# Kernel tuning notes

Measured on AMD Instinct MI355X. Metric: run time of the kernel, lower is better.

Reference implementation:

```python
import jax, jax.numpy as jnp
import numpy as np

SIZE = 32
NUM_CLASSES = 10
B = 16384
RTOL = 0.01
ATOL = 0.01
MAX_STEPS = 96
H0 = 0.05


def setup_inputs() -> dict:
    key = jax.random.key(0)
    ks = jax.random.split(key, 9)
    p = lambda k, s: 0.1 * jax.random.normal(k, s, dtype=jnp.float32)
    z = lambda n: jnp.zeros((n,), dtype=jnp.float32)
    x = jax.random.normal(ks[0], (B, 2), dtype=jnp.float32)
    # per-sample ODE end times T_i in (0, 3]
    samples = 3.0 * jax.random.uniform(ks[1], (B, 1), dtype=jnp.float32) + 1e-3
    return dict(
        x=x, samples=samples,
        node_w1=p(ks[2], (3, SIZE)), node_b1=z(SIZE),
        node_w2=p(ks[3], (SIZE, SIZE)), node_b2=z(SIZE),
        node_w3=p(ks[4], (SIZE, 2)), node_b3=z(2),
        fc_w=p(ks[5], (2, NUM_CLASSES)), fc_b=z(NUM_CLASSES),
        enc_w1=p(ks[6], (2, SIZE)), enc_b1=z(SIZE),
        enc_w2=p(ks[7], (SIZE, SIZE)), enc_b2=z(SIZE),
        enc_w3=p(ks[8], (SIZE, 2)), enc_b3=z(2),
    )


def _net_forward(x, samples, node_w1, node_b1, node_w2, node_b2, node_w3, node_b3,
                 fc_w, fc_b, enc_w1, enc_b1, enc_w2, enc_b2, enc_w3, enc_b3):
    # Encoder -> (alpha, beta) feed only the external prob_model (no effect on act_vec)
    h = jax.nn.relu(x @ enc_w1 + enc_b1)
    h = jax.nn.relu(h @ enc_w2 + enc_b2)
    ab = h @ enc_w3 + enc_b3
    alpha, beta = jnp.exp(ab[:, 0]), jnp.exp(ab[:, 1])  # unused downstream (side effects only)

    # samples[samples >= 50] = 50
    T = jnp.minimum(samples[:, 0], 50.0)  # [B] per-sample end times

    def f(t, y):  # NODE dynamics; t: [B], y: [B,2]
        zin = jnp.concatenate([t[:, None], y], axis=1)  # [B,3]
        h1 = jax.nn.relu(zin @ node_w1 + node_b1)
        h2 = jax.nn.relu(h1 @ node_w2 + node_b2)
        return h2 @ node_w3 + node_b3  # [B,2]

    def step(carry, _):
        t, y, hstep = carry
        rem = T - t
        active = rem > 1e-8
        hs = jnp.where(active, jnp.minimum(hstep, rem), 0.0)  # never overshoot T
        hb = hs[:, None]
        # Dopri5 (RK45) stages
        k1 = f(t, y)
        k2 = f(t + hs * 0.2, y + hb * (0.2 * k1))
        k3 = f(t + hs * 0.3, y + hb * (3.0 / 40.0 * k1 + 9.0 / 40.0 * k2))
        k4 = f(t + hs * 0.8, y + hb * (44.0 / 45.0 * k1 - 56.0 / 15.0 * k2 + 32.0 / 9.0 * k3))
        k5 = f(t + hs * (8.0 / 9.0), y + hb * (19372.0 / 6561.0 * k1 - 25360.0 / 2187.0 * k2 + 64448.0 / 6561.0 * k3 - 212.0 / 729.0 * k4))
        k6 = f(t + hs, y + hb * (9017.0 / 3168.0 * k1 - 355.0 / 33.0 * k2 + 46732.0 / 5247.0 * k3 + 49.0 / 176.0 * k4 - 5103.0 / 18656.0 * k5))
        y5 = y + hb * (35.0 / 384.0 * k1 + 500.0 / 1113.0 * k3 + 125.0 / 192.0 * k4 - 2187.0 / 6784.0 * k5 + 11.0 / 84.0 * k6)
        k7 = f(t + hs, y5)
        err = hb * (71.0 / 57600.0 * k1 - 71.0 / 16695.0 * k3 + 71.0 / 1920.0 * k4 - 17253.0 / 339200.0 * k5 + 22.0 / 525.0 * k6 - 1.0 / 40.0 * k7)
        scale = ATOL + RTOL * jnp.maximum(jnp.abs(y), jnp.abs(y5))
        en = jnp.sqrt(jnp.mean((err / scale) ** 2, axis=1))  # [B]
        accept = active & (en <= 1.0)
        fac = jnp.clip(0.9 * jnp.maximum(en, 1e-10) ** (-0.2), 0.2, 10.0)
        t_n = jnp.where(accept, t + hs, t)
        y_n = jnp.where(accept[:, None], y5, y)
        h_n = jnp.where(active, hs * fac, hstep)
        return (t_n, y_n, h_n), None

    t0 = jnp.zeros((x.shape[0],), dtype=x.dtype)
    h0 = jnp.full((x.shape[0],), H0, dtype=x.dtype)
    (tF, yF, hF), _ = jax.lax.scan(step, (t0, x, h0), None, length=MAX_STEPS)

    # temp[idx] = flow of x[idx] from t=0 to its own T[idx] (sort/scatter in the
    # original only routes each sample's own interpolated state back to its row)
    act = yF @ fc_w + fc_b  # [B, num_classes]
    return act[None, :, :]  # act_vec: [1, B, num_classes]


def reference(x, samples, node_w1, node_b1, node_w2, node_b2, node_w3, node_b3,
              fc_w, fc_b, enc_w1, enc_b1, enc_w2, enc_b2, enc_w3, enc_b3):
    return _net_forward(x, samples, node_w1, node_b1, node_w2, node_b2, node_w3, node_b3,
                        fc_w, fc_b, enc_w1, enc_b1, enc_w2, enc_b2, enc_w3, enc_b3)
```

## Files before the change

### kernel.cpp

```cpp
#include <hip/hip_runtime.h>
#include <math.h>


#define MAXS 96

typedef float v2f __attribute__((ext_vector_type(2)));

static __device__ __forceinline__ v2f splat(float s){ v2f v; v.x=s; v.y=s; return v; }
static __device__ __forceinline__ v2f vfma(v2f a, v2f b, v2f c){ return __builtin_elementwise_fma(a,b,c); }
static __device__ __forceinline__ v2f vrelu(v2f a){ return __builtin_elementwise_max(a, splat(0.0f)); }
static __device__ __forceinline__ v2f slo(v2f v){ return __builtin_shufflevector(v,v,0,0); }
static __device__ __forceinline__ v2f shi(v2f v){ return __builtin_shufflevector(v,v,1,1); }

template<int CTRL>
static __device__ __forceinline__ float dppf(float x){
    return __int_as_float(__builtin_amdgcn_update_dpp(0, __float_as_int(x), CTRL, 0xF, 0xF, false));
}
static __device__ __forceinline__ v2f dpp_allreduce16(v2f p){
    p.x += dppf<0xB1>(p.x);  p.y += dppf<0xB1>(p.y);
    p.x += dppf<0x4E>(p.x);  p.y += dppf<0x4E>(p.y);
    p.x += dppf<0x141>(p.x); p.y += dppf<0x141>(p.y);
    p.x += dppf<0x140>(p.x); p.y += dppf<0x140>(p.y);
    return p;
}

__global__ __launch_bounds__(256, 2) void node_kernel(
    const float* __restrict__ x, const float* __restrict__ samples,
    const float* __restrict__ w1, const float* __restrict__ b1,
    const float* __restrict__ w2, const float* __restrict__ b2,
    const float* __restrict__ w3, const float* __restrict__ b3,
    const float* __restrict__ fcw, const float* __restrict__ fcb,
    float* __restrict__ out, int n)
{
    const int tid = blockIdx.x * blockDim.x + threadIdx.x;
    const int gid = tid >> 4;
    const int m   = tid & 15;
    const int eA  = 2 * gid, eB = 2 * gid + 1;
    if (eA >= n) return;
    const bool hasB = (eB < n);

    __shared__ float lds[16 * 68];
    float* slot = &lds[(threadIdx.x >> 4) * 68];

    const v2f* w2v = (const v2f*)w2;
    v2f w2c[32];
#pragma unroll
    for (int j = 0; j < 32; ++j) w2c[j] = w2v[j * 16 + m];

    v2f w1s00 = splat(w1[ 0 + 2*m]), w1s01 = splat(w1[ 0 + 2*m + 1]);
    v2f w1s10 = splat(w1[32 + 2*m]), w1s11 = splat(w1[32 + 2*m + 1]);
    v2f w1s20 = splat(w1[64 + 2*m]), w1s21 = splat(w1[64 + 2*m + 1]);
    v2f b1s0  = splat(b1[2*m]),      b1s1  = splat(b1[2*m + 1]);
    v2f b2s0  = splat(b2[2*m]),      b2s1  = splat(b2[2*m + 1]);
    v2f w3s00 = splat(w3[(2*m)*2+0]),   w3s01 = splat(w3[(2*m)*2+1]);
    v2f w3s10 = splat(w3[(2*m+1)*2+0]), w3s11 = splat(w3[(2*m+1)*2+1]);
    v2f b3s0  = splat(b3[0]),        b3s1  = splat(b3[1]);

#pragma unroll
    for (int j = 0; j < 32; ++j) { asm volatile("" : "+v"(w2c[j])); }
    asm volatile("" : "+v"(w1s00), "+v"(w1s01), "+v"(w1s10), "+v"(w1s11));
    asm volatile("" : "+v"(w1s20), "+v"(w1s21), "+v"(b1s0), "+v"(b1s1));
    asm volatile("" : "+v"(b2s0), "+v"(b2s1));
    asm volatile("" : "+v"(w3s00), "+v"(w3s01), "+v"(w3s10), "+v"(w3s11));

    v2f xA = ((const v2f*)x)[eA];
    v2f xB = hasB ? ((const v2f*)x)[eB] : xA;
    v2f y0pk; y0pk.x = xA.x; y0pk.y = xB.x;
    v2f y1pk; y1pk.x = xA.y; y1pk.y = xB.y;
    float TA = fminf(samples[eA], 50.0f);
    float TB = hasB ? fminf(samples[eB], 50.0f) : TA;
    v2f tpk = splat(0.0f);
    v2f hpk = splat(0.05f);

    auto f_eval = [&](v2f tt, v2f z0, v2f z1, v2f& o0, v2f& o1) {
        v2f hc0 = vrelu(vfma(tt, w1s00, vfma(z0, w1s10, vfma(z1, w1s20, b1s0))));
        v2f hc1 = vrelu(vfma(tt, w1s01, vfma(z0, w1s11, vfma(z1, w1s21, b1s1))));
        float4 wv; wv.x = hc0.x; wv.y = hc0.y; wv.z = hc1.x; wv.w = hc1.y;
        ((float4*)slot)[m] = wv;
        const float4* gp = (const float4*)slot;
        v2f a0 = b2s0, a1 = splat(0.0f), a2 = b2s1, a3 = splat(0.0f);
#pragma unroll
        for (int j = 0; j < 16; ++j) {
            float4 r = gp[j];
            v2f pA; pA.x = r.x; pA.y = r.y;
            v2f pB; pB.x = r.z; pB.y = r.w;
            a0 = vfma(pA, slo(w2c[2*j]),     a0);
            a2 = vfma(pA, shi(w2c[2*j]),     a2);
            a1 = vfma(pB, slo(w2c[2*j + 1]), a1);
            a3 = vfma(pB, shi(w2c[2*j + 1]), a3);
        }
        v2f h20 = vrelu(a0 + a1);
        v2f h21 = vrelu(a2 + a3);
        v2f p0 = vfma(h20, w3s00, h21 * w3s10);
        v2f p1 = vfma(h20, w3s01, h21 * w3s11);
        p0 = dpp_allreduce16(p0);
        p1 = dpp_allreduce16(p1);
        o0 = p0 + b3s0;
        o1 = p1 + b3s1;
    };

    v2f k10, k11; f_eval(tpk, y0pk, y1pk, k10, k11);

    for (int s = 0; s < MAXS; ++s) {
        float remA = TA - tpk.x, remB = TB - tpk.y;
        bool actA = remA > 1e-8f;
        bool actB = hasB && (remB > 1e-8f);
        if (!actA && !actB) break;
        float hsA = actA ? fminf(hpk.x, remA) : 0.0f;
        float hsB = actB ? fminf(hpk.y, remB) : 0.0f;
        v2f hb; hb.x = hsA; hb.y = hsB;

        v2f k20,k21,k30,k31,k40,k41,k50,k51,k60,k61,k70,k71,u0,u1,y50,y51;

        u0 = vfma(hb, splat(0.2f) * k10, y0pk);
        u1 = vfma(hb, splat(0.2f) * k11, y1pk);
        f_eval(tpk + hb * splat(0.2f), u0, u1, k20, k21);

        u0 = vfma(hb, vfma(splat((float)(3.0/40.0)), k10, splat((float)(9.0/40.0)) * k20), y0pk);
        u1 = vfma(hb, vfma(splat((float)(3.0/40.0)), k11, splat((float)(9.0/40.0)) * k21), y1pk);
        f_eval(tpk + hb * splat(0.3f), u0, u1, k30, k31);

        u0 = vfma(hb, vfma(splat((float)(44.0/45.0)), k10,
                  vfma(splat((float)(-56.0/15.0)), k20, splat((float)(32.0/9.0)) * k30)), y0pk);
        u1 = vfma(hb, vfma(splat((float)(44.0/45.0)), k11,
                  vfma(splat((float)(-56.0/15.0)), k21, splat((float)(32.0/9.0)) * k31)), y1pk);
        f_eval(tpk + hb * splat(0.8f), u0, u1, k40, k41);

        u0 = vfma(hb, vfma(splat((float)(19372.0/6561.0)), k10,
                  vfma(splat((float)(-25360.0/2187.0)), k20,
                  vfma(splat((float)(64448.0/6561.0)), k30,
                       splat((float)(-212.0/729.0)) * k40))), y0pk);
        u1 = vfma(hb, vfma(splat((float)(19372.0/6561.0)), k11,
                  vfma(splat((float)(-25360.0/2187.0)), k21,
                  vfma(splat((float)(64448.0/6561.0)), k31,
                       splat((float)(-212.0/729.0)) * k41))), y1pk);
        f_eval(tpk + hb * splat((float)(8.0/9.0)), u0, u1, k50, k51);

        u0 = vfma(hb, vfma(splat((float)(9017.0/3168.0)), k10,
                  vfma(splat((float)(-355.0/33.0)), k20,
                  vfma(splat((float)(46732.0/5247.0)), k30,
                  vfma(splat((float)(49.0/176.0)), k40,
                       splat((float)(-5103.0/18656.0)) * k50)))), y0pk);
        u1 = vfma(hb, vfma(splat((float)(9017.0/3168.0)), k11,
                  vfma(splat((float)(-355.0/33.0)), k21,
                  vfma(splat((float)(46732.0/5247.0)), k31,
                  vfma(splat((float)(49.0/176.0)), k41,
                       splat((float)(-5103.0/18656.0)) * k51)))), y1pk);
        f_eval(tpk + hb, u0, u1, k60, k61);

        y50 = vfma(hb, vfma(splat((float)(35.0/384.0)), k10,
                   vfma(splat((float)(500.0/1113.0)), k30,
                   vfma(splat((float)(125.0/192.0)), k40,
                   vfma(splat((float)(-2187.0/6784.0)), k50,
                        splat((float)(11.0/84.0)) * k60)))), y0pk);
        y51 = vfma(hb, vfma(splat((float)(35.0/384.0)), k11,
                   vfma(splat((float)(500.0/1113.0)), k31,
                   vfma(splat((float)(125.0/192.0)), k41,
                   vfma(splat((float)(-2187.0/6784.0)), k51,
                        splat((float)(11.0/84.0)) * k61)))), y1pk);
        f_eval(tpk + hb, y50, y51, k70, k71);

        v2f err0 = hb * vfma(splat((float)(71.0/57600.0)), k10,
                        vfma(splat((float)(-71.0/16695.0)), k30,
                        vfma(splat((float)(71.0/1920.0)), k40,
                        vfma(splat((float)(-17253.0/339200.0)), k50,
                        vfma(splat((float)(22.0/525.0)), k60,
                             splat((float)(-1.0/40.0)) * k70)))));
        v2f err1 = hb * vfma(splat((float)(71.0/57600.0)), k11,
                        vfma(splat((float)(-71.0/16695.0)), k31,
                        vfma(splat((float)(71.0/1920.0)), k41,
                        vfma(splat((float)(-17253.0/339200.0)), k51,
                        vfma(splat((float)(22.0/525.0)), k61,
                             splat((float)(-1.0/40.0)) * k71)))));

        v2f sc0 = vfma(splat(0.01f),
                  __builtin_elementwise_max(__builtin_elementwise_abs(y0pk),
                                            __builtin_elementwise_abs(y50)), splat(0.01f));
        v2f sc1 = vfma(splat(0.01f),
                  __builtin_elementwise_max(__builtin_elementwise_abs(y1pk),
                                            __builtin_elementwise_abs(y51)), splat(0.01f));
        v2f r0 = err0 / sc0;
        v2f r1 = err1 / sc1;

        float enA = sqrtf(0.5f * (r0.x * r0.x + r1.x * r1.x));
        float enB = sqrtf(0.5f * (r0.y * r0.y + r1.y * r1.y));
        float facA = fminf(fmaxf(0.9f * exp2f(-0.2f * log2f(fmaxf(enA, 1e-10f))), 0.2f), 10.0f);
        float facB = fminf(fmaxf(0.9f * exp2f(-0.2f * log2f(fmaxf(enB, 1e-10f))), 0.2f), 10.0f);

        bool accA = actA && (enA <= 1.0f);
        bool accB = actB && (enB <= 1.0f);
        if (accA) { tpk.x += hsA; y0pk.x = y50.x; y1pk.x = y51.x; k10.x = k70.x; k11.x = k71.x; }
        if (accB) { tpk.y += hsB; y0pk.y = y50.y; y1pk.y = y51.y; k10.y = k70.y; k11.y = k71.y; }
        if (actA) hpk.x = hsA * facA;
        if (actB) hpk.y = hsB * facB;
    }

    if (m < 10) {
        out[10 * eA + m] = fmaf(y0pk.x, fcw[m], fmaf(y1pk.x, fcw[10 + m], fcb[m]));
        if (hasB)
            out[10 * eB + m] = fmaf(y0pk.y, fcw[m], fmaf(y1pk.y, fcw[10 + m], fcb[m]));
    }
}

extern "C" void kernel_launch(void* const* d_in, const int* in_sizes, int n_in,
                              void* d_out, int out_size, void* d_ws, size_t ws_size,
                              hipStream_t stream) {
    const float* x   = (const float*)d_in[0];
    const float* sm  = (const float*)d_in[1];
    const float* w1  = (const float*)d_in[2];
    const float* b1  = (const float*)d_in[3];
    const float* w2  = (const float*)d_in[4];
    const float* b2  = (const float*)d_in[5];
    const float* w3  = (const float*)d_in[6];
    const float* b3  = (const float*)d_in[7];
    const float* fcw = (const float*)d_in[8];
    const float* fcb = (const float*)d_in[9];
    float* out = (float*)d_out;

    int n = in_sizes[1];
    const int block = 256;
    long long groups  = (n + 1) / 2;
    long long threads = groups * 16;
    int grid = (int)((threads + block - 1) / block);
    node_kernel<<<grid, block, 0, stream>>>(x, sm, w1, b1, w2, b2, w3, b3,
                                            fcw, fcb, out, n);
}
```

Before: 105.2 us.

## Replace LDS hidden-layer exchange with DPP butterfly broadcast across 16 lanes

The first-layer activations are no longer written to shared memory and read back by every lane of the 16-lane group. They are now spread across lanes with a DPP butterfly of xor-style permutations, and the W2 rows are pre-permuted per lane so each received value lines up with the right weight. This removes the LDS store/load round trips and their waits from every f evaluation. In exchange each evaluation issues 60 DPP moves and needs more live registers for the g0/g1 arrays, which could limit occupancy.

```diff
diff --git a/kernel.cpp b/kernel.cpp
--- a/kernel.cpp
+++ b/kernel.cpp
@@ -39,29 +39,28 @@
     if (eA >= n) return;
     const bool hasB = (eB < n);
 
-    __shared__ float lds[16 * 68];
-    float* slot = &lds[(threadIdx.x >> 4) * 68];
+    const int P[16] = {0,1,2,3, 7,6,5,4, 15,14,13,12, 8,9,10,11};
 
     const v2f* w2v = (const v2f*)w2;
-    v2f w2c[32];
+    v2f w2a[16], w2b[16];
 #pragma unroll
-    for (int j = 0; j < 32; ++j) w2c[j] = w2v[j * 16 + m];
-
-    v2f w1s00 = splat(w1[ 0 + 2*m]), w1s01 = splat(w1[ 0 + 2*m + 1]);
-    v2f w1s10 = splat(w1[32 + 2*m]), w1s11 = splat(w1[32 + 2*m + 1]);
-    v2f w1s20 = splat(w1[64 + 2*m]), w1s21 = splat(w1[64 + 2*m + 1]);
-    v2f b1s0  = splat(b1[2*m]),      b1s1  = splat(b1[2*m + 1]);
-    v2f b2s0  = splat(b2[2*m]),      b2s1  = splat(b2[2*m + 1]);
-    v2f w3s00 = splat(w3[(2*m)*2+0]),   w3s01 = splat(w3[(2*m)*2+1]);
-    v2f w3s10 = splat(w3[(2*m+1)*2+0]), w3s11 = splat(w3[(2*m+1)*2+1]);
-    v2f b3s0  = splat(b3[0]),        b3s1  = splat(b3[1]);
+    for (int i = 0; i < 16; ++i) {
+        int j = m ^ P[i];
+        w2a[i] = w2v[(2*j    ) * 16 + m];
+        w2b[i] = w2v[(2*j + 1) * 16 + m];
+    }
+    const v2f* w1v = (const v2f*)w1;
+    v2f w1p0 = w1v[0*16 + m], w1p1 = w1v[1*16 + m], w1p2 = w1v[2*16 + m];
+    v2f b1p  = ((const v2f*)b1)[m];
+    v2f b2p  = ((const v2f*)b2)[m];
+    v2f w3p0; w3p0.x = w3[(2*m)*2+0]; w3p0.y = w3[(2*m+1)*2+0];
+    v2f w3p1; w3p1.x = w3[(2*m)*2+1]; w3p1.y = w3[(2*m+1)*2+1];
+    v2f b3c  = { b3[0], b3[1] };
 
 #pragma unroll
-    for (int j = 0; j < 32; ++j) { asm volatile("" : "+v"(w2c[j])); }
-    asm volatile("" : "+v"(w1s00), "+v"(w1s01), "+v"(w1s10), "+v"(w1s11));
-    asm volatile("" : "+v"(w1s20), "+v"(w1s21), "+v"(b1s0), "+v"(b1s1));
-    asm volatile("" : "+v"(b2s0), "+v"(b2s1));
-    asm volatile("" : "+v"(w3s00), "+v"(w3s01), "+v"(w3s10), "+v"(w3s11));
+    for (int i = 0; i < 16; ++i) { asm volatile("" : "+v"(w2a[i]), "+v"(w2b[i])); }
+    asm volatile("" : "+v"(w1p0), "+v"(w1p1), "+v"(w1p2), "+v"(b1p), "+v"(b2p));
+    asm volatile("" : "+v"(w3p0), "+v"(w3p1));
 
     v2f xA = ((const v2f*)x)[eA];
     v2f xB = hasB ? ((const v2f*)x)[eB] : xA;
@@ -73,30 +72,37 @@
     v2f hpk = splat(0.05f);
 
     auto f_eval = [&](v2f tt, v2f z0, v2f z1, v2f& o0, v2f& o1) {
-        v2f hc0 = vrelu(vfma(tt, w1s00, vfma(z0, w1s10, vfma(z1, w1s20, b1s0))));
-        v2f hc1 = vrelu(vfma(tt, w1s01, vfma(z0, w1s11, vfma(z1, w1s21, b1s1))));
-        float4 wv; wv.x = hc0.x; wv.y = hc0.y; wv.z = hc1.x; wv.w = hc1.y;
-        ((float4*)slot)[m] = wv;
-        const float4* gp = (const float4*)slot;
-        v2f a0 = b2s0, a1 = splat(0.0f), a2 = b2s1, a3 = splat(0.0f);
+        v2f h0 = vrelu(vfma(tt, slo(w1p0), vfma(z0, slo(w1p1), vfma(z1, slo(w1p2), slo(b1p)))));
+        v2f h1 = vrelu(vfma(tt, shi(w1p0), vfma(z0, shi(w1p1), vfma(z1, shi(w1p2), shi(b1p)))));
+
+        v2f g0[16], g1[16];
+        g0[0] = h0; g1[0] = h1;
+#define BF(d,s,C) g0[d].x=dppf<C>(g0[s].x); g0[d].y=dppf<C>(g0[s].y); \
+                  g1[d].x=dppf<C>(g1[s].x); g1[d].y=dppf<C>(g1[s].y);
+        BF(1,0,0xB1)
+        BF(2,0,0x4E)  BF(3,1,0x4E)
+        BF(4,0,0x141) BF(5,1,0x141) BF(6,2,0x141) BF(7,3,0x141)
+        BF(8,0,0x140) BF(9,1,0x140) BF(10,2,0x140) BF(11,3,0x140)
+        BF(12,4,0x140) BF(13,5,0x140) BF(14,6,0x140) BF(15,7,0x140)
+#undef BF
+
+        v2f a0 = slo(b2p), a1 = shi(b2p), c0 = splat(0.0f), c1 = splat(0.0f);
 #pragma unroll
-        for (int j = 0; j < 16; ++j) {
-            float4 r = gp[j];
-            v2f pA; pA.x = r.x; pA.y = r.y;
-            v2f pB; pB.x = r.z; pB.y = r.w;
-            a0 = vfma(pA, slo(w2c[2*j]),     a0);
-            a2 = vfma(pA, shi(w2c[2*j]),     a2);
-            a1 = vfma(pB, slo(w2c[2*j + 1]), a1);
-            a3 = vfma(pB, shi(w2c[2*j + 1]), a3);
+        for (int i = 0; i < 16; ++i) {
+            a0 = vfma(g0[i], slo(w2a[i]), a0);
+            a1 = vfma(g0[i], shi(w2a[i]), a1);
+            c0 = vfma(g1[i], slo(w2b[i]), c0);
+            c1 = vfma(g1[i], shi(w2b[i]), c1);
         }
-        v2f h20 = vrelu(a0 + a1);
-        v2f h21 = vrelu(a2 + a3);
-        v2f p0 = vfma(h20, w3s00, h21 * w3s10);
-        v2f p1 = vfma(h20, w3s01, h21 * w3s11);
+        v2f h2a = vrelu(a0 + c0);
+        v2f h2b = vrelu(a1 + c1);
+
+        v2f p0 = vfma(h2a, slo(w3p0), h2b * shi(w3p0));
+        v2f p1 = vfma(h2a, slo(w3p1), h2b * shi(w3p1));
         p0 = dpp_allreduce16(p0);
         p1 = dpp_allreduce16(p1);
-        o0 = p0 + b3s0;
-        o1 = p1 + b3s1;
+        o0 = p0 + slo(b3c);
+        o1 = p1 + shi(b3c);
     };
 
     v2f k10, k11; f_eval(tpk, y0pk, y1pk, k10, k11);
```

New measurement: 114.4 us. 1.09x slower.
